# Optimization experiments

Measured on AMD Instinct MI355X. Metric: run time of the kernel, lower is better.

The kernel has to match this reference:

```python
import jax, jax.numpy as jnp
import numpy as np

NUM_HEADS = 12
WS = 8
ROPE_BASE = 100.0  # croco/dust3r RoPE2D default frequency base


def _rope1d(t, p, inv_freq):
    # t: [Bw, h, N, d], p: [Bw, N], inv_freq: [d/2]
    freqs = p[..., None] * inv_freq                      # [Bw, N, d/2]
    emb = jnp.concatenate([freqs, freqs], axis=-1)       # [Bw, N, d]
    cos = jnp.cos(emb)[:, None, :, :]
    sin = jnp.sin(emb)[:, None, :, :]
    t1, t2 = jnp.split(t, 2, axis=-1)
    rot = jnp.concatenate([-t2, t1], axis=-1)            # rotate_half
    return t * cos + rot * sin


def _rope2d(tokens, pos):
    # tokens: [Bw, h, N, D], pos: [Bw, N, 2] (y, x). First D/2 dims use y, last D/2 use x.
    D = tokens.shape[-1]
    d = D // 2
    inv_freq = 1.0 / (ROPE_BASE ** (jnp.arange(0, d, 2, dtype=jnp.float32) / d))
    ty, tx = jnp.split(tokens, 2, axis=-1)
    return jnp.concatenate([_rope1d(ty, pos[..., 0], inv_freq),
                            _rope1d(tx, pos[..., 1], inv_freq)], axis=-1)


def setup_inputs() -> dict:
    B, H, W, C = 16, 64, 64, 768
    key = jax.random.key(0)
    ks = jax.random.split(key, 7)
    x_img = jax.random.normal(ks[0], (B, H * W, C), dtype=jnp.float32)
    yy, xx = jnp.meshgrid(jnp.arange(H), jnp.arange(W), indexing='ij')
    pos = jnp.stack([yy, xx], axis=-1).reshape(1, H * W, 2).astype(jnp.float32)
    pos2d_img = jnp.broadcast_to(pos, (B, H * W, 2))
    unseen = jax.random.normal(ks[1], (B, C), dtype=jnp.float32)
    sc = C ** -0.5
    qkv_w = jax.random.normal(ks[2], (3 * C, C), dtype=jnp.float32) * sc
    qkv_b = jax.random.normal(ks[3], (3 * C,), dtype=jnp.float32) * 0.02
    proj_w = jax.random.normal(ks[4], (C, C), dtype=jnp.float32) * sc
    proj_b = jax.random.normal(ks[5], (C,), dtype=jnp.float32) * 0.02
    return {'x_img': x_img, 'pos2d_img': pos2d_img, 'unseen': unseen,
            'qkv_w': qkv_w, 'qkv_b': qkv_b, 'proj_w': proj_w, 'proj_b': proj_b,
            'H': H, 'W': W}


def reference(x_img, pos2d_img, unseen, qkv_w, qkv_b, proj_w, proj_b, H, W):
    B, HW, C = x_img.shape
    hd = C // NUM_HEADS
    scale = hd ** -0.5
    nWh, nWw = H // WS, W // WS
    Bwin, Nwin = B * nWh * nWw, WS * WS

    # window partition
    xw = x_img.reshape(B, nWh, WS, nWw, WS, C).transpose(0, 1, 3, 2, 4, 5).reshape(Bwin, Nwin, C)
    pw = pos2d_img.reshape(B, nWh, WS, nWw, WS, 2).transpose(0, 1, 3, 2, 4, 5).reshape(Bwin, Nwin, 2)

    # append unseen token (shared across windows of an image)
    u = jnp.broadcast_to(unseen[:, None, None, :], (B, nWh * nWw, 1, C)).reshape(Bwin, 1, C)
    xw = jnp.concatenate([xw, u], axis=1)                # [Bwin, Nwin+1, C]

    qkv = xw @ qkv_w.T + qkv_b                           # [Bwin, N, 3C]
    qkv = qkv.reshape(Bwin, Nwin + 1, 3, NUM_HEADS, hd)
    q = qkv[:, :, 0].transpose(0, 2, 1, 3)               # [Bwin, h, N, hd]
    k = qkv[:, :, 1].transpose(0, 2, 1, 3)
    v = qkv[:, :, 2].transpose(0, 2, 1, 3)

    # RoPE2D on image tokens only; unseen token gets no RoPE
    q = jnp.concatenate([_rope2d(q[:, :, :Nwin], pw), q[:, :, Nwin:]], axis=2)
    k = jnp.concatenate([_rope2d(k[:, :, :Nwin], pw), k[:, :, Nwin:]], axis=2)

    attn = jax.nn.softmax(jnp.einsum('bhqd,bhkd->bhqk', q, k) * scale, axis=-1)
    out = jnp.einsum('bhqk,bhkd->bhqd', attn, v)
    out = out.transpose(0, 2, 1, 3).reshape(Bwin, Nwin + 1, C)
    out = out @ proj_w.T + proj_b

    # window merge
    out_img = out[:, :Nwin].reshape(B, nWh, nWw, WS, WS, C).transpose(0, 1, 3, 2, 4, 5).reshape(B, HW, C)
    out_unseen = out[:, Nwin].reshape(B, nWh * nWw, C).mean(axis=1)  # [B, C]
    return out_img, out_unseen
```

## Files before the change

kernel.cpp:

```cpp
#include <hip/hip_runtime.h>
#include <cstdint>
#include <cstddef>

typedef __attribute__((ext_vector_type(8)))  __bf16 bf16x8;
typedef __attribute__((ext_vector_type(4)))  float  f32x4;
typedef __attribute__((ext_vector_type(2)))  unsigned int u32x2;

#define DI __device__ __forceinline__

constexpr int Cdim = 768;
constexpr int C3   = 2304;
constexpr int NT   = 65;
constexpr int ROWS = 1024 * NT;
constexpr int ROWS_PAD = ROWS + 32;
constexpr int TP   = 96;
constexpr int PS   = 128;
constexpr long long OUT_IMG = 16LL * 4096 * 768;

DI float bf2f(unsigned short u) { unsigned int x = (unsigned int)u << 16; float f; __builtin_memcpy(&f, &x, 4); return f; }
DI unsigned short f2bf(float f) { unsigned int x; __builtin_memcpy(&x, &f, 4); x = x + 0x7fffu + ((x >> 16) & 1u); return (unsigned short)(x >> 16); }

DI void gload_lds16(const unsigned short* g, unsigned short* l) {
  __builtin_amdgcn_global_load_lds((__attribute__((address_space(1))) void*)g,
                                   (__attribute__((address_space(3))) void*)l, 16, 0, 0);
}

__global__ void k_prep(const float* __restrict__ qkv_w, const float* __restrict__ proj_w,
                       unsigned short* __restrict__ wqb, unsigned short* __restrict__ wpb,
                       float* __restrict__ rope) {
  const int NW1 = 2304 * 768;
  const int NW2 = 768 * 768;
  int total = NW1 + NW2 + 1024;
  for (int i = blockIdx.x * blockDim.x + threadIdx.x; i < total; i += gridDim.x * blockDim.x) {
    if (i < NW1) wqb[i] = f2bf(qkv_w[i]);
    else if (i < NW1 + NW2) wpb[i - NW1] = f2bf(proj_w[i - NW1]);
    else {
      int e = i - NW1 - NW2;
      int p = e >> 4, j = e & 15;
      float inv = powf(100.f, -(float)j * (1.f / 16.f));
      float a = (float)p * inv;
      rope[2 * e]     = cosf(a);
      rope[2 * e + 1] = sinf(a);
    }
  }
}

__global__ void k_xw(const float* __restrict__ x, const float* __restrict__ unseen,
                     unsigned short* __restrict__ xw) {
  int row = blockIdx.x;
  int w = row / NT, t = row - w * NT;
  const float* src;
  if (t == 64) {
    src = unseen + (size_t)(w >> 6) * Cdim;
  } else {
    int wy = (w >> 3) & 7, wx = w & 7;
    int hw = ((wy << 3) + (t >> 3)) * 64 + (wx << 3) + (t & 7);
    src = x + ((size_t)(w >> 6) * 4096 + hw) * Cdim;
  }
  float4 v = ((const float4*)src)[threadIdx.x];
  unsigned int u0 = (unsigned)f2bf(v.x) | ((unsigned)f2bf(v.y) << 16);
  unsigned int u1 = (unsigned)f2bf(v.z) | ((unsigned)f2bf(v.w) << 16);
  ((u32x2*)(xw + (size_t)row * Cdim))[threadIdx.x] = (u32x2){u0, u1};
}

template<int MODE, int NTILES>
__global__ __launch_bounds__(512, 2) void k_gemm(
    const unsigned short* __restrict__ A, const unsigned short* __restrict__ Bw,
    const float* __restrict__ bias, const float* __restrict__ rope,
    unsigned short* __restrict__ Cb, float* __restrict__ outp) {
  constexpr int K = 768;
  constexpr int NK = K / 32;
  constexpr int BUF = 16384;
  __shared__ alignas(16) unsigned short lds[4 * BUF];

  constexpr int nwg = 260 * NTILES;
  constexpr int q8 = nwg / 8, r8 = nwg % 8;
  int id = blockIdx.x;
  int xcd = id & 7, lid = id >> 3;
  int wg = (xcd < r8 ? xcd * (q8 + 1) : r8 * (q8 + 1) + (xcd - r8) * q8) + lid;
  int mtile = wg / NTILES, ntile = wg - mtile * NTILES;
  int m0 = mtile * 256, n0 = ntile * 256;

  int tid = threadIdx.x;
  int lane = tid & 63, wid = tid >> 6;
  int lq = lane & 15, lg = lane >> 4;
  int wm = (wid >> 2) * 128;
  int wn = (wid & 3) * 64;

  auto stageA = [&](int tt) {
    unsigned short* d = lds + (tt & 3) * BUF;
    int k0 = tt * 32;
    #pragma unroll
    for (int c = 0; c < 2; ++c) {
      int chunk = c * 512 + tid;
      gload_lds16(A + (size_t)(m0 + (chunk >> 2)) * K + k0 + (chunk & 3) * 8,
                  d + (size_t)(c * 512 + (tid & ~63)) * 8);
    }
  };
  auto stageB = [&](int tt) {
    unsigned short* d = lds + (tt & 3) * BUF + 8192;
    int k0 = tt * 32;
    #pragma unroll
    for (int c = 0; c < 2; ++c) {
      int chunk = c * 512 + tid;
      gload_lds16(Bw + (size_t)(n0 + (chunk >> 2)) * K + k0 + (chunk & 3) * 8,
                  d + (size_t)(c * 512 + (tid & ~63)) * 8);
    }
  };

  f32x4 acc[8][4];
  #pragma unroll
  for (int i = 0; i < 8; ++i)
    #pragma unroll
    for (int j = 0; j < 4; ++j) acc[i][j] = (f32x4){0.f, 0.f, 0.f, 0.f};

  stageA(0); stageB(0);
  stageA(1); stageB(1);
  stageA(2); stageB(2);
  asm volatile("s_waitcnt vmcnt(8)\n\ts_barrier" ::: "memory");

  for (int t = 0; t < NK; ++t) {
    const unsigned short* sA = lds + (t & 3) * BUF;
    const unsigned short* sB = sA + 8192;
    int tp = t + 3;

    bf16x8 bfr[4], af[4];
    #pragma unroll
    for (int nf = 0; nf < 4; ++nf)
      bfr[nf] = *(const bf16x8*)(sB + (wn + nf * 16 + lq) * 32 + lg * 8);
    #pragma unroll
    for (int mf = 0; mf < 4; ++mf)
      af[mf] = *(const bf16x8*)(sA + (wm + mf * 16 + lq) * 32 + lg * 8);
    if (tp < NK) stageA(tp);
    __builtin_amdgcn_s_setprio(1);
    #pragma unroll
    for (int mf = 0; mf < 4; ++mf)
      #pragma unroll
      for (int nf = 0; nf < 4; ++nf)
        acc[mf][nf] = __builtin_amdgcn_mfma_f32_16x16x32_bf16(af[mf], bfr[nf], acc[mf][nf], 0, 0, 0);
    __builtin_amdgcn_s_setprio(0);

    bf16x8 af2[4];
    #pragma unroll
    for (int mf = 0; mf < 4; ++mf)
      af2[mf] = *(const bf16x8*)(sA + (wm + 64 + mf * 16 + lq) * 32 + lg * 8);
    if (tp < NK) stageB(tp);
    __builtin_amdgcn_s_setprio(1);
    #pragma unroll
    for (int mf = 0; mf < 4; ++mf)
      #pragma unroll
      for (int nf = 0; nf < 4; ++nf)
        acc[4 + mf][nf] = __builtin_amdgcn_mfma_f32_16x16x32_bf16(af2[mf], bfr[nf], acc[4 + mf][nf], 0, 0, 0);
    __builtin_amdgcn_s_setprio(0);

    if (t < NK - 1) {
      if (t <= NK - 4)      asm volatile("s_waitcnt vmcnt(8)\n\ts_barrier" ::: "memory");
      else if (t == NK - 3) asm volatile("s_waitcnt vmcnt(4)\n\ts_barrier" ::: "memory");
      else                  asm volatile("s_waitcnt vmcnt(0)\n\ts_barrier" ::: "memory");
    }
  }

  #pragma unroll
  for (int mf = 0; mf < 8; ++mf) {
    #pragma unroll
    for (int r = 0; r < 4; ++r) {
      int row = m0 + wm + mf * 16 + (lg << 2) + r;
      int w = row / NT, t = row - w * NT;
      int wy = (w >> 3) & 7, wx = w & 7;
      int py = (wy << 3) + (t >> 3), px = (wx << 3) + (t & 7);
      #pragma unroll
      for (int a = 0; a < 2; ++a) {
        int col0 = n0 + wn + a * 32 + lq;
        int col1 = col0 + 16;
        float v0 = acc[mf][2 * a][r] + bias[col0];
        float v1 = acc[mf][2 * a + 1][r] + bias[col1];
        if (MODE == 0) {
          if (col0 < 1536 && t != 64) {
            int p = a ? px : py;
            const float* rp = rope + ((p << 4) + lq) * 2;
            float cc = rp[0], ss = rp[1];
            float o0 = v0 * cc - v1 * ss;
            float o1 = v1 * cc + v0 * ss;
            v0 = o0; v1 = o1;
          }
          unsigned short* cr = Cb + (size_t)row * C3;
          cr[col0] = f2bf(v0);
          cr[col1] = f2bf(v1);
        } else {
          if (t == 64) {
            float* ub = outp + OUT_IMG + (size_t)(w >> 6) * Cdim;
            atomicAdd(ub + col0, v0 * (1.f / 64.f));
            atomicAdd(ub + col1, v1 * (1.f / 64.f));
          } else {
            float* orow = outp + ((size_t)(w >> 6) * 4096 + py * 64 + px) * Cdim;
            orow[col0] = v0;
            orow[col1] = v1;
          }
        }
      }
    }
  }
}

__global__ void k_vt(const unsigned short* __restrict__ qkv, unsigned short* __restrict__ Vt) {
  int bh = blockIdx.x;
  int w = bh / 12, h = bh - w * 12;
  __shared__ float sv[65][65];
  const unsigned short* base = qkv + (size_t)w * NT * C3 + 1536 + h * 64;
  for (int i = threadIdx.x; i < 65 * 64; i += 256) {
    int t = i >> 6, d = i & 63;
    sv[t][d] = bf2f(base[(size_t)t * C3 + d]);
  }
  __syncthreads();
  unsigned short* out = Vt + (size_t)bh * 64 * TP;
  for (int i = threadIdx.x; i < 64 * TP; i += 256) {
    int d = i / TP, t = i - d * TP;
    out[i] = f2bf(t < 65 ? sv[t][d] : 0.f);
  }
}

__global__ __launch_bounds__(64) void k_attn(const unsigned short* __restrict__ qkv,
                                             const unsigned short* __restrict__ Vt,
                                             unsigned short* __restrict__ att) {
  __shared__ alignas(16) unsigned short P[80 * PS];
  int h = blockIdx.x, w = blockIdx.y;
  int lane = threadIdx.x;
  int lq = lane & 15, lg = lane >> 4;

  const unsigned short* qb = qkv + (size_t)w * NT * C3 + h * 64;
  const unsigned short* kb = qb + 768;

  bf16x8 kf[5][2];
  #pragma unroll
  for (int kt = 0; kt < 5; ++kt)
    #pragma unroll
    for (int ks = 0; ks < 2; ++ks)
      kf[kt][ks] = *(const bf16x8*)(kb + (size_t)(kt * 16 + lq) * C3 + ks * 32 + lg * 8);

  const unsigned short* vb = Vt + (size_t)(w * 12 + h) * 64 * TP;
  bf16x8 vf[3][4];
  #pragma unroll
  for (int ks = 0; ks < 3; ++ks)
    #pragma unroll
    for (int dt = 0; dt < 4; ++dt)
      vf[ks][dt] = *(const bf16x8*)(vb + (size_t)(dt * 16 + lq) * TP + ks * 32 + lg * 8);

  for (int i = lane; i < 80 * 8; i += 64) {
    int row = i >> 3, j = i & 7;
    int byteo = row * (PS * 2) + 160 + j * 4;
    byteo ^= (row & 7) << 4;
    *(unsigned int*)((char*)P + byteo) = 0u;
  }

  #pragma unroll 1
  for (int qt = 0; qt < 5; ++qt) {
    bf16x8 qf[2];
    #pragma unroll
    for (int ks = 0; ks < 2; ++ks)
      qf[ks] = *(const bf16x8*)(qb + (size_t)(qt * 16 + lq) * C3 + ks * 32 + lg * 8);

    f32x4 sa[5];
    #pragma unroll
    for (int kt = 0; kt < 5; ++kt) {
      sa[kt] = (f32x4){0.f, 0.f, 0.f, 0.f};
      #pragma unroll
      for (int ks = 0; ks < 2; ++ks)
        sa[kt] = __builtin_amdgcn_mfma_f32_16x16x32_bf16(kf[kt][ks], qf[ks], sa[kt], 0, 0, 0);
    }
    float pv[5][4];
    float m = -1e30f;
    #pragma unroll
    for (int kt = 0; kt < 5; ++kt)
      #pragma unroll
      for (int r = 0; r < 4; ++r) {
        int tok = kt * 16 + lg * 4 + r;
        float s = sa[kt][r] * 0.125f;
        bool ok = tok < 65;
        pv[kt][r] = ok ? s : -1e30f;
        m = (ok && s > m) ? s : m;
      }
    m = fmaxf(m, __shfl_xor(m, 16));
    m = fmaxf(m, __shfl_xor(m, 32));
    float sum = 0.f;
    #pragma unroll
    for (int kt = 0; kt < 5; ++kt)
      #pragma unroll
      for (int r = 0; r < 4; ++r) {
        float e = (pv[kt][r] > -1e29f) ? exp2f((pv[kt][r] - m) * 1.44269504f) : 0.f;
        pv[kt][r] = e;
        sum += e;
      }
    sum += __shfl_xor(sum, 16);
    sum += __shfl_xor(sum, 32);
    float rinv = 1.f / sum;

    int q = qt * 16 + lq;
    #pragma unroll
    for (int kt = 0; kt < 5; ++kt) {
      unsigned int u0 = (unsigned)f2bf(pv[kt][0] * rinv) | ((unsigned)f2bf(pv[kt][1] * rinv) << 16);
      unsigned int u1 = (unsigned)f2bf(pv[kt][2] * rinv) | ((unsigned)f2bf(pv[kt][3] * rinv) << 16);
      int byteo = q * (PS * 2) + kt * 32 + lg * 8;
      byteo ^= (q & 7) << 4;
      *(u32x2*)((char*)P + byteo) = (u32x2){u0, u1};
    }
    asm volatile("s_waitcnt lgkmcnt(0)" ::: "memory");

    bf16x8 bp[3];
    #pragma unroll
    for (int ks = 0; ks < 3; ++ks) {
      int byteo = q * (PS * 2) + ks * 64 + lg * 16;
      byteo ^= (q & 7) << 4;
      bp[ks] = *(const bf16x8*)((char*)P + byteo);
    }
    #pragma unroll
    for (int dt = 0; dt < 4; ++dt) {
      f32x4 o = (f32x4){0.f, 0.f, 0.f, 0.f};
      #pragma unroll
      for (int ks = 0; ks < 3; ++ks)
        o = __builtin_amdgcn_mfma_f32_16x16x32_bf16(vf[ks][dt], bp[ks], o, 0, 0, 0);
      if (q < 65) {
        unsigned int u0 = (unsigned)f2bf(o[0]) | ((unsigned)f2bf(o[1]) << 16);
        unsigned int u1 = (unsigned)f2bf(o[2]) | ((unsigned)f2bf(o[3]) << 16);
        *(u32x2*)(att + (size_t)(w * NT + q) * Cdim + h * 64 + dt * 16 + lg * 4) = (u32x2){u0, u1};
      }
    }
  }
}

extern "C" void kernel_launch(void* const* d_in, const int* in_sizes, int n_in,
                              void* d_out, int out_size, void* d_ws, size_t ws_size,
                              hipStream_t stream) {
  const float* x_img  = (const float*)d_in[0];
  const float* unseen = (const float*)d_in[2];
  const float* qkv_w  = (const float*)d_in[3];
  const float* qkv_b  = (const float*)d_in[4];
  const float* proj_w = (const float*)d_in[5];
  const float* proj_b = (const float*)d_in[6];

  char* ws = (char*)d_ws;
  size_t off = 0;
  auto alloc = [&](size_t bytes) { void* p = ws + off; off = (off + bytes + 255) & ~(size_t)255; return p; };
  unsigned short* xw  = (unsigned short*)alloc((size_t)ROWS * Cdim * 2);
  unsigned short* qkv = (unsigned short*)alloc((size_t)ROWS_PAD * C3 * 2);
  unsigned short* Vt  = (unsigned short*)alloc((size_t)12288 * 64 * TP * 2);
  unsigned short* wqb = (unsigned short*)alloc((size_t)C3 * Cdim * 2);
  unsigned short* wpb = (unsigned short*)alloc((size_t)Cdim * Cdim * 2);
  float* rope = (float*)alloc(64 * 16 * 2 * sizeof(float));

  hipMemsetAsync((float*)d_out + OUT_IMG, 0, 16 * Cdim * sizeof(float), stream);

  k_prep<<<512, 256, 0, stream>>>(qkv_w, proj_w, wqb, wpb, rope);
  k_xw<<<ROWS, 192, 0, stream>>>(x_img, unseen, xw);
  k_gemm<0, 9><<<260 * 9, 512, 0, stream>>>(xw, wqb, qkv_b, rope, qkv, nullptr);
  k_vt<<<12288, 256, 0, stream>>>(qkv, Vt);
  k_attn<<<dim3(12, 1024), 64, 0, stream>>>(qkv, Vt, xw);
  k_gemm<1, 3><<<260 * 3, 512, 0, stream>>>(xw, wpb, proj_b, nullptr, nullptr, (float*)d_out);
}
```

Measured before the change: 686.2 us.

## Restructure GEMM mainloop with 64-wide K tiles, swizzled LDS, and phased staging

The bf16 GEMM main loop moves from a 4-deep ring of 32-wide K tiles to 64-wide K tiles. A is double-buffered one tile ahead and B is staged two tiles ahead. LDS rows are XOR-swizzled to avoid bank conflicts, and each K tile is split into four MFMA phases, with global-to-LDS loads and extra barriers placed between phases so memory traffic overlaps with compute. This halves the number of loop iterations and reduces LDS conflicts, but adds more barriers per tile and a more fragile buffer-reuse scheme that depends on barrier ordering.

```diff
diff --git a/kernel.cpp b/kernel.cpp
--- a/kernel.cpp
+++ b/kernel.cpp
@@ -69,9 +69,8 @@
     const float* __restrict__ bias, const float* __restrict__ rope,
     unsigned short* __restrict__ Cb, float* __restrict__ outp) {
   constexpr int K = 768;
-  constexpr int NK = K / 32;
-  constexpr int BUF = 16384;
-  __shared__ alignas(16) unsigned short lds[4 * BUF];
+  constexpr int NK = K / 64;
+  __shared__ alignas(16) unsigned short lds[65536];
 
   constexpr int nwg = 260 * NTILES;
   constexpr int q8 = nwg / 8, r8 = nwg % 8;
@@ -87,25 +86,34 @@
   int wm = (wid >> 2) * 128;
   int wn = (wid & 3) * 64;
 
-  auto stageA = [&](int tt) {
-    unsigned short* d = lds + (tt & 3) * BUF;
-    int k0 = tt * 32;
-    #pragma unroll
-    for (int c = 0; c < 2; ++c) {
-      int chunk = c * 512 + tid;
-      gload_lds16(A + (size_t)(m0 + (chunk >> 2)) * K + k0 + (chunk & 3) * 8,
-                  d + (size_t)(c * 512 + (tid & ~63)) * 8);
-    }
-  };
-  auto stageB = [&](int tt) {
-    unsigned short* d = lds + (tt & 3) * BUF + 8192;
-    int k0 = tt * 32;
-    #pragma unroll
-    for (int c = 0; c < 2; ++c) {
-      int chunk = c * 512 + tid;
-      gload_lds16(Bw + (size_t)(n0 + (chunk >> 2)) * K + k0 + (chunk & 3) * 8,
-                  d + (size_t)(c * 512 + (tid & ~63)) * 8);
-    }
+  int srow0 = wid * 8 + (lane >> 3);
+  int skc   = (lane & 7) ^ (lane >> 3);
+  auto stage = [&](const unsigned short* G, int off0, int k0, int h, unsigned short* base) {
+    #pragma unroll
+    for (int j = 0; j < 2; ++j) {
+      int row = h * 128 + j * 64 + srow0;
+      gload_lds16(G + (size_t)(off0 + row) * K + k0 + skc * 8,
+                  base + h * 8192 + (j * 8 + wid) * 512);
+    }
+  };
+
+  auto rd8 = [&](bf16x8* dst, const unsigned short* s, int rbase) {
+    #pragma unroll
+    for (int f = 0; f < 4; ++f)
+      #pragma unroll
+      for (int ks = 0; ks < 2; ++ks) {
+        int row = rbase + f * 16 + lq;
+        dst[f * 2 + ks] = *(const bf16x8*)(s + row * 64 + (((ks * 4 + lg) ^ (lq & 7)) * 8));
+      }
+  };
+  auto rd4 = [&](bf16x8* dst, const unsigned short* s, int rbase) {
+    #pragma unroll
+    for (int f = 0; f < 2; ++f)
+      #pragma unroll
+      for (int ks = 0; ks < 2; ++ks) {
+        int row = rbase + f * 16 + lq;
+        dst[f * 2 + ks] = *(const bf16x8*)(s + row * 64 + (((ks * 4 + lg) ^ (lq & 7)) * 8));
+      }
   };
 
   f32x4 acc[8][4];
@@ -114,51 +122,78 @@
     #pragma unroll
     for (int j = 0; j < 4; ++j) acc[i][j] = (f32x4){0.f, 0.f, 0.f, 0.f};
 
-  stageA(0); stageB(0);
-  stageA(1); stageB(1);
-  stageA(2); stageB(2);
-  asm volatile("s_waitcnt vmcnt(8)\n\ts_barrier" ::: "memory");
-
-  for (int t = 0; t < NK; ++t) {
-    const unsigned short* sA = lds + (t & 3) * BUF;
-    const unsigned short* sB = sA + 8192;
-    int tp = t + 3;
-
-    bf16x8 bfr[4], af[4];
-    #pragma unroll
-    for (int nf = 0; nf < 4; ++nf)
-      bfr[nf] = *(const bf16x8*)(sB + (wn + nf * 16 + lq) * 32 + lg * 8);
+  bf16x8 af[8], b01[4], b23[4];
+
+  #define BARR() __builtin_amdgcn_s_barrier()
+  #define LGKM0() do { asm volatile("s_waitcnt lgkmcnt(0)" ::: "memory"); \
+                       __builtin_amdgcn_sched_barrier(0); } while (0)
+
+  auto mfma16 = [&](bf16x8* a4, bf16x8* b2, int mb, int nb) {
+    __builtin_amdgcn_s_setprio(1);
     #pragma unroll
     for (int mf = 0; mf < 4; ++mf)
-      af[mf] = *(const bf16x8*)(sA + (wm + mf * 16 + lq) * 32 + lg * 8);
-    if (tp < NK) stageA(tp);
-    __builtin_amdgcn_s_setprio(1);
-    #pragma unroll
-    for (int mf = 0; mf < 4; ++mf)
-      #pragma unroll
-      for (int nf = 0; nf < 4; ++nf)
-        acc[mf][nf] = __builtin_amdgcn_mfma_f32_16x16x32_bf16(af[mf], bfr[nf], acc[mf][nf], 0, 0, 0);
+      #pragma unroll
+      for (int nf = 0; nf < 2; ++nf)
+        #pragma unroll
+        for (int ks = 0; ks < 2; ++ks)
+          acc[mb + mf][nb + nf] =
+            __builtin_amdgcn_mfma_f32_16x16x32_bf16(a4[mf * 2 + ks], b2[nf * 2 + ks],
+                                                    acc[mb + mf][nb + nf], 0, 0, 0);
     __builtin_amdgcn_s_setprio(0);
-
-    bf16x8 af2[4];
-    #pragma unroll
-    for (int mf = 0; mf < 4; ++mf)
-      af2[mf] = *(const bf16x8*)(sA + (wm + 64 + mf * 16 + lq) * 32 + lg * 8);
-    if (tp < NK) stageB(tp);
-    __builtin_amdgcn_s_setprio(1);
-    #pragma unroll
-    for (int mf = 0; mf < 4; ++mf)
-      #pragma unroll
-      for (int nf = 0; nf < 4; ++nf)
-        acc[4 + mf][nf] = __builtin_amdgcn_mfma_f32_16x16x32_bf16(af2[mf], bfr[nf], acc[4 + mf][nf], 0, 0, 0);
-    __builtin_amdgcn_s_setprio(0);
-
-    if (t < NK - 1) {
-      if (t <= NK - 4)      asm volatile("s_waitcnt vmcnt(8)\n\ts_barrier" ::: "memory");
-      else if (t == NK - 3) asm volatile("s_waitcnt vmcnt(4)\n\ts_barrier" ::: "memory");
-      else                  asm volatile("s_waitcnt vmcnt(0)\n\ts_barrier" ::: "memory");
-    }
-  }
+  };
+
+  auto tile = [&](int T, bool doA, bool doB, int endcnt) {
+    const unsigned short* sA = lds + (T & 1) * 16384;
+    const unsigned short* sB = lds + 32768 + (T & 1) * 16384;
+    unsigned short* dA = lds + ((T + 1) & 1) * 16384;
+    unsigned short* dB = lds + 32768 + (T & 1) * 16384;
+
+    rd8(af, sA, wm);
+    rd4(b01, sB, wn);
+    if (doA) stage(A, m0, (T + 1) * 64, 0, dA);
+    BARR(); LGKM0();
+    mfma16(af, b01, 0, 0);
+    BARR();
+
+    rd4(b23, sB, wn + 32);
+    if (doA) stage(A, m0, (T + 1) * 64, 1, dA);
+    BARR(); LGKM0();
+    mfma16(af, b23, 0, 2);
+    BARR();
+
+    rd8(af + 0, sA, wm + 64);
+    if (doB) stage(Bw, n0, (T + 2) * 64, 0, dB);
+    BARR(); LGKM0();
+    mfma16(af, b23, 4, 2);
+    BARR();
+
+    if (doB) stage(Bw, n0, (T + 2) * 64, 1, dB);
+    BARR();
+    mfma16(af, b01, 4, 0);
+    if (endcnt == 4) asm volatile("s_waitcnt vmcnt(4)" ::: "memory");
+    else if (endcnt == 0) asm volatile("s_waitcnt vmcnt(0)" ::: "memory");
+    if (endcnt >= 0) BARR();
+  };
+
+  {
+    unsigned short* a0 = lds;
+    unsigned short* b0 = lds + 32768;
+    unsigned short* b1 = lds + 32768 + 16384;
+    stage(A, m0, 0, 0, a0); stage(A, m0, 0, 1, a0);
+    stage(Bw, n0, 0, 0, b0); stage(Bw, n0, 0, 1, b0);
+    stage(Bw, n0, 64, 0, b1); stage(Bw, n0, 64, 1, b1);
+    asm volatile("s_waitcnt vmcnt(4)" ::: "memory");
+    BARR();
+  }
+
+  #pragma unroll 2
+  for (int T = 0; T < NK - 2; ++T)
+    tile(T, true, true, 4);
+  tile(NK - 2, true, false, 0);
+  tile(NK - 1, false, false, -1);
+
+  #undef BARR
+  #undef LGKM0
 
   #pragma unroll
   for (int mf = 0; mf < 8; ++mf) {
```

Measured after the change: 681.1 us. No clear change (-0.7%).
